# Kernel optimization log

Measured on AMD Instinct MI355X. Metric: run time of the kernel, lower is better.

Reference implementation:

```python
import jax, jax.numpy as jnp
import numpy as np

EPS = 1e-6

def _avgpool(x, k):
    # AvgPool2d(kernel_size=k, stride=k) for divisible H, W
    B, C, H, W = x.shape
    return x.reshape(B, C, H // k, k, W // k, k).mean(axis=(3, 5))

def setup_inputs() -> dict:
    key = jax.random.key(0)
    ks = jax.random.split(key, 5)
    B, C, H, W, kern = 32, 128, 32, 32, 2
    shp = (B, C, H, W)
    return {
        "mu_a_": jax.random.normal(ks[0], shp, dtype=jnp.float32),
        "logvar_a_": jax.random.normal(ks[1], shp, dtype=jnp.float32),
        "mu_b_": jax.random.normal(ks[2], shp, dtype=jnp.float32),
        "logvar_b_": jax.random.normal(ks[3], shp, dtype=jnp.float32),
        "eps": jax.random.normal(ks[4], (B, C, H // kern, W // kern), dtype=jnp.float32),
        "kern": kern,
    }

def _log_mean_density(z, mu, var):
    # z: [B,C,h,w] (one MC sample per batch row i); mu/var: [B,C,h,w]
    # pairwise unnormalized Gaussian density ratio, mean over the mixture (j) axis
    d = jnp.exp(-(z[:, None] - mu[None]) ** 2 / (2.0 * var[None])) / jnp.sqrt(var[None])  # [B,B,C,h,w]
    return jnp.log(jnp.mean(d, axis=1) + EPS)  # [B,C,h,w]

def reference(mu_a_, logvar_a_, mu_b_, logvar_b_, eps, kern):
    k = int(kern)
    mu_a = _avgpool(mu_a_, k)
    mu_b = _avgpool(mu_b_, k)
    var_a = _avgpool(jnp.exp(logvar_a_), k) / (k * k)
    var_b = _avgpool(jnp.exp(logvar_b_), k) / (k * k)
    z = mu_a + jnp.sqrt(var_a) * eps  # reparameterized MC samples, one per row
    term = _log_mean_density(z, mu_a, var_a) - _log_mean_density(z, mu_b, var_b)  # [B,C,h,w]
    # torch loop adds each per-i term (shape [C,h,w]) broadcast into a [B,C,h,w]
    # accumulator, then sums -> equals B * sum_i,c,h,w term
    B = mu_a.shape[0]
    return jnp.asarray(B, term.dtype) * jnp.sum(term)
```

## Files before the change

kernel.cpp:

```cpp
#include <hip/hip_runtime.h>


#define GKL_EPS 1e-6f

__global__ __launch_bounds__(256) void gkl_main(
    const float* __restrict__ muA, const float* __restrict__ lvA,
    const float* __restrict__ muB, const float* __restrict__ lvB,
    const float* __restrict__ eps, double* __restrict__ ws)
{
    __shared__ float sh[2*1028 + 32*17 + 4];

    const int bid = blockIdx.x;
    const int c   = bid >> 4;
    const int h   = bid & 15;
    const int t   = threadIdx.x;
    const int w   = t & 15;
    const int b0  = t >> 4;
    const int row0 = 2*h, col0 = 2*w;

    #pragma unroll
    for (int rep = 0; rep < 2; ++rep) {
        const int b = b0 + rep*16;
        const size_t base = ((size_t)(b*128 + c)*32 + row0)*32 + col0;
        const int qidx = ((b >> 1)*16 + w)*4 + (b & 1)*2;

        float2 m0 = *(const float2*)(muA + base);
        float2 m1 = *(const float2*)(muA + base + 32);
        float2 l0 = *(const float2*)(lvA + base);
        float2 l1 = *(const float2*)(lvA + base + 32);
        float mu  = (m0.x + m0.y + m1.x + m1.y) * 0.25f;
        float var = (__expf(l0.x) + __expf(l0.y) + __expf(l1.x) + __expf(l1.y)) * 0.0625f;
        float s   = __builtin_amdgcn_sqrtf(0.72134752f * __builtin_amdgcn_rcpf(var));
        *(float2*)(sh + qidx) = make_float2(s, mu);
        float ev = eps[((b*128 + c)*16 + h)*16 + w];
        sh[2*1028 + b*17 + w] = fmaf(__builtin_amdgcn_sqrtf(var), ev, mu);

        float2 n0 = *(const float2*)(muB + base);
        float2 n1 = *(const float2*)(muB + base + 32);
        float2 k0 = *(const float2*)(lvB + base);
        float2 k1 = *(const float2*)(lvB + base + 32);
        float mub  = (n0.x + n0.y + n1.x + n1.y) * 0.25f;
        float varb = (__expf(k0.x) + __expf(k0.y) + __expf(k1.x) + __expf(k1.y)) * 0.0625f;
        float sb   = __builtin_amdgcn_sqrtf(0.72134752f * __builtin_amdgcn_rcpf(varb));
        *(float2*)(sh + 1028 + qidx) = make_float2(sb, mub);
    }
    __syncthreads();

    const int lane = t & 63;
    const int wv   = t >> 6;
    const int i    = lane & 31;
    const int side = lane >> 5;
    const float4* __restrict__ Qs = (const float4*)(sh + side*1028);
    const float* __restrict__ zp  = sh + 2*1028;
    float* __restrict__ wsum      = sh + 2*1028 + 32*17;

    float tot = 0.f;
    #pragma unroll
    for (int q = 0; q < 4; ++q) {
        const int p  = wv*4 + q;
        const float zi = zp[i*17 + p];
        float acc0 = 0.f, acc1 = 0.f;
        #pragma unroll
        for (int jj = 0; jj < 16; ++jj) {
            float4 f = Qs[jj*16 + p];
            float d0 = zi - f.y, d1 = zi - f.w;
            float s0 = f.x,      s1 = f.z;
            acc0 = fmaf(s0, exp2f(-(d0*d0*(s0*s0))), acc0);
            acc1 = fmaf(s1, exp2f(-(d1*d1*(s1*s1))), acc1);
        }
        float lg = __logf(fmaf(acc0 + acc1, 0.036794063f, GKL_EPS));
        tot += side ? -lg : lg;
    }

    #pragma unroll
    for (int o = 32; o; o >>= 1) tot += __shfl_xor(tot, o, 64);
    if (lane == 0) wsum[wv] = tot;
    __syncthreads();
    if (t == 0)
        ws[bid] = (double)wsum[0] + (double)wsum[1] + (double)wsum[2] + (double)wsum[3];
}

__global__ __launch_bounds__(256) void gkl_final(
    const double* __restrict__ ws, float* __restrict__ out)
{
    __shared__ double part[4];
    const int t = threadIdx.x;
    double s = 0.0;
    for (int k = t; k < 2048; k += 256) s += ws[k];
    #pragma unroll
    for (int o = 32; o; o >>= 1) s += __shfl_xor(s, o, 64);
    if ((t & 63) == 0) part[t >> 6] = s;
    __syncthreads();
    if (t == 0) out[0] = (float)(32.0 * (part[0] + part[1] + part[2] + part[3]));
}

extern "C" void kernel_launch(void* const* d_in, const int* in_sizes, int n_in,
                              void* d_out, int out_size, void* d_ws, size_t ws_size,
                              hipStream_t stream) {
    const float* muA = (const float*)d_in[0];
    const float* lvA = (const float*)d_in[1];
    const float* muB = (const float*)d_in[2];
    const float* lvB = (const float*)d_in[3];
    const float* ep  = (const float*)d_in[4];
    double* ws = (double*)d_ws;
    float* out = (float*)d_out;

    gkl_main<<<2048, 256, 0, stream>>>(muA, lvA, muB, lvB, ep, ws);
    gkl_final<<<1, 256, 0, stream>>>(ws, out);
}
```

Baseline: 123.2 us.

## Split each (c,h) row across two blocks and restructure shared-memory layout

Each block now handles half of a (c,h) row (8 w positions), doubling the grid to 4096 blocks so each thread loads one batch element instead of two. The shared-memory layout is reorganized per-w with mu and scale packed together, and the inner loop processes two w positions per wave over all 32 mixture components. The scale is computed with rsq and folded so the exponent is a single square. The intent is more parallelism, shorter per-thread load phases and fewer ALU ops, at the cost of more blocks and partial sums for the final reduction.

```diff
diff --git a/kernel.cpp b/kernel.cpp
--- a/kernel.cpp
+++ b/kernel.cpp
@@ -8,41 +8,41 @@
     const float* __restrict__ muB, const float* __restrict__ lvB,
     const float* __restrict__ eps, double* __restrict__ ws)
 {
-    __shared__ float sh[2*1028 + 32*17 + 4];
+    __shared__ float sh[2720];
+    __shared__ float wsum[4];
 
     const int bid = blockIdx.x;
-    const int c   = bid >> 4;
-    const int h   = bid & 15;
+    const int c   = bid >> 5;
+    const int h   = (bid >> 1) & 15;
+    const int wh  = bid & 1;
     const int t   = threadIdx.x;
-    const int w   = t & 15;
-    const int b0  = t >> 4;
-    const int row0 = 2*h, col0 = 2*w;
+    const int b   = t >> 3;
+    const int wl  = t & 7;
+    const int w   = wh*8 + wl;
 
-    #pragma unroll
-    for (int rep = 0; rep < 2; ++rep) {
-        const int b = b0 + rep*16;
-        const size_t base = ((size_t)(b*128 + c)*32 + row0)*32 + col0;
-        const int qidx = ((b >> 1)*16 + w)*4 + (b & 1)*2;
+    {
+        const int base = ((b*128 + c)*32 + 2*h)*32 + 2*w;
 
         float2 m0 = *(const float2*)(muA + base);
         float2 m1 = *(const float2*)(muA + base + 32);
         float2 l0 = *(const float2*)(lvA + base);
         float2 l1 = *(const float2*)(lvA + base + 32);
-        float mu  = (m0.x + m0.y + m1.x + m1.y) * 0.25f;
-        float var = (__expf(l0.x) + __expf(l0.y) + __expf(l1.x) + __expf(l1.y)) * 0.0625f;
-        float s   = __builtin_amdgcn_sqrtf(0.72134752f * __builtin_amdgcn_rcpf(var));
-        *(float2*)(sh + qidx) = make_float2(s, mu);
-        float ev = eps[((b*128 + c)*16 + h)*16 + w];
-        sh[2*1028 + b*17 + w] = fmaf(__builtin_amdgcn_sqrtf(var), ev, mu);
-
         float2 n0 = *(const float2*)(muB + base);
         float2 n1 = *(const float2*)(muB + base + 32);
         float2 k0 = *(const float2*)(lvB + base);
         float2 k1 = *(const float2*)(lvB + base + 32);
+        float ev  = eps[((b*128 + c)*16 + h)*16 + w];
+
+        float mu  = (m0.x + m0.y + m1.x + m1.y) * 0.25f;
+        float var = (__expf(l0.x)+__expf(l0.y)+__expf(l1.x)+__expf(l1.y)) * 0.0625f;
+        float rs  = __builtin_amdgcn_rsqf(var);
+        *(float2*)(sh + wl*68 + 2*b) = make_float2(mu, 0.84932185f * rs);
+        sh[2176 + b*17 + wl] = fmaf(var * rs, ev, mu);
+
         float mub  = (n0.x + n0.y + n1.x + n1.y) * 0.25f;
-        float varb = (__expf(k0.x) + __expf(k0.y) + __expf(k1.x) + __expf(k1.y)) * 0.0625f;
-        float sb   = __builtin_amdgcn_sqrtf(0.72134752f * __builtin_amdgcn_rcpf(varb));
-        *(float2*)(sh + 1028 + qidx) = make_float2(sb, mub);
+        float varb = (__expf(k0.x)+__expf(k0.y)+__expf(k1.x)+__expf(k1.y)) * 0.0625f;
+        float rsb  = __builtin_amdgcn_rsqf(varb);
+        *(float2*)(sh + 1092 + wl*68 + 2*b) = make_float2(mub, 0.84932185f * rsb);
     }
     __syncthreads();
 
@@ -50,27 +50,28 @@
     const int wv   = t >> 6;
     const int i    = lane & 31;
     const int side = lane >> 5;
-    const float4* __restrict__ Qs = (const float4*)(sh + side*1028);
-    const float* __restrict__ zp  = sh + 2*1028;
-    float* __restrict__ wsum      = sh + 2*1028 + 32*17;
+    const float* __restrict__ qp0 = sh + side*1092 + (wv*2)*68;
+    const float* __restrict__ qp1 = qp0 + 68;
+    const float z0 = sh[2176 + i*17 + wv*2];
+    const float z1 = sh[2176 + i*17 + wv*2 + 1];
 
-    float tot = 0.f;
+    float acc0 = 0.f, acc1 = 0.f;
     #pragma unroll
-    for (int q = 0; q < 4; ++q) {
-        const int p  = wv*4 + q;
-        const float zi = zp[i*17 + p];
-        float acc0 = 0.f, acc1 = 0.f;
-        #pragma unroll
-        for (int jj = 0; jj < 16; ++jj) {
-            float4 f = Qs[jj*16 + p];
-            float d0 = zi - f.y, d1 = zi - f.w;
-            float s0 = f.x,      s1 = f.z;
-            acc0 = fmaf(s0, exp2f(-(d0*d0*(s0*s0))), acc0);
-            acc1 = fmaf(s1, exp2f(-(d1*d1*(s1*s1))), acc1);
-        }
-        float lg = __logf(fmaf(acc0 + acc1, 0.036794063f, GKL_EPS));
-        tot += side ? -lg : lg;
+    for (int k = 0; k < 16; ++k) {
+        float4 f = *(const float4*)(qp0 + 4*k);
+        float4 g = *(const float4*)(qp1 + 4*k);
+        float d0 = z0 - f.x, e0 = d0 * f.y;
+        acc0 = fmaf(f.y, exp2f(-(e0*e0)), acc0);
+        float d1 = z0 - f.z, e1 = d1 * f.w;
+        acc0 = fmaf(f.w, exp2f(-(e1*e1)), acc0);
+        float d2 = z1 - g.x, e2 = d2 * g.y;
+        acc1 = fmaf(g.y, exp2f(-(e2*e2)), acc1);
+        float d3 = z1 - g.z, e3 = d3 * g.w;
+        acc1 = fmaf(g.w, exp2f(-(e3*e3)), acc1);
     }
+    float lg = __logf(fmaf(acc0, 0.036794063f, GKL_EPS))
+             + __logf(fmaf(acc1, 0.036794063f, GKL_EPS));
+    float tot = side ? -lg : lg;
 
     #pragma unroll
     for (int o = 32; o; o >>= 1) tot += __shfl_xor(tot, o, 64);
@@ -86,7 +87,7 @@
     __shared__ double part[4];
     const int t = threadIdx.x;
     double s = 0.0;
-    for (int k = t; k < 2048; k += 256) s += ws[k];
+    for (int k = t; k < 4096; k += 256) s += ws[k];
     #pragma unroll
     for (int o = 32; o; o >>= 1) s += __shfl_xor(s, o, 64);
     if ((t & 63) == 0) part[t >> 6] = s;
@@ -105,6 +106,6 @@
     double* ws = (double*)d_ws;
     float* out = (float*)d_out;
 
-    gkl_main<<<2048, 256, 0, stream>>>(muA, lvA, muB, lvB, ep, ws);
+    gkl_main<<<4096, 256, 0, stream>>>(muA, lvA, muB, lvB, ep, ws);
     gkl_final<<<1, 256, 0, stream>>>(ws, out);
 }
```

Result: no change. 122.0 us (-1.0%).
